# Kernel optimization log

Measured on AMD Instinct MI355X. Metric: run time of the kernel, lower is better.

## Reference

```python
import jax, jax.numpy as jnp
import numpy as np

BATCH = 2048
NUM_FIELDS = 32
EMBED = 64
NPAIRS = NUM_FIELDS * (NUM_FIELDS - 1) // 2  # 496
# static pair indices (i < j), same order as the torch double loop
ROW, COL = np.triu_indices(NUM_FIELDS, k=1)
ROW = jnp.asarray(ROW)
COL = jnp.asarray(COL)


def setup_inputs() -> dict:
    key = jax.random.key(0)
    k1, k2 = jax.random.split(key)
    emb_inputs = jax.random.normal(k1, (BATCH, NUM_FIELDS, EMBED), dtype=jnp.float32)
    # xavier_normal_ on kernel of shape (E, NC2, E): fan_in = NC2*E (dims[1:]), fan_out = E*E... 
    # torch: fan_in = size(1)*receptive = NPAIRS*EMBED? torch uses size(1)*prod(size[2:]) = NPAIRS*EMBED,
    # fan_out = size(0)*prod(size[2:]) = EMBED*EMBED; std = sqrt(2/(fan_in+fan_out))
    fan_in = NPAIRS * EMBED
    fan_out = EMBED * EMBED
    std = float(np.sqrt(2.0 / (fan_in + fan_out)))
    kernel = jax.random.normal(k2, (EMBED, NPAIRS, EMBED), dtype=jnp.float32) * std
    return {"emb_inputs": emb_inputs, "kernel": kernel}


def reference(emb_inputs, kernel):
    # emb_inputs: (B, N, E); kernel: (E, NC2, E)
    p = emb_inputs[:, ROW]  # (B, NC2, E)
    q = emb_inputs[:, COL]  # (B, NC2, E)
    # torch: kp[b,i,pair] = sum_j p[b,pair,j] * kernel[i,pair,j]; out[b,pair] = sum_i kp*q
    kp = jnp.einsum('bpj,ipj->bpi', p, kernel)  # (B, NC2, E) -- avoids (B,E,NC2,E) blowup
    outputs = jnp.sum(kp * q, axis=-1)          # (B, NC2)
    return outputs[:, None, :]                  # (B, 1, NC2)
```

## Files before the change

kernel.cpp:

```cpp
#include <hip/hip_runtime.h>
#include <hip/hip_bf16.h>
#include <math.h>

#define BATCH   2048
#define NFIELDS 32
#define EMBED   64
#define NPAIRS  496

typedef __attribute__((ext_vector_type(8))) short bf16x8;
typedef __attribute__((ext_vector_type(4))) float f32x4;

__device__ __forceinline__ unsigned short f2bf(float x) {
    unsigned int u = __float_as_uint(x);
    unsigned int r = 0x7fffu + ((u >> 16) & 1u);
    return (unsigned short)((u + r) >> 16);
}
__device__ __forceinline__ float bf2f(unsigned short b) {
    return __uint_as_float(((unsigned int)b) << 16);
}
__device__ __forceinline__ bf16x8 cvt8(const float* p) {
    float4 v0 = *(const float4*)p;
    float4 v1 = *(const float4*)(p + 4);
    bf16x8 o;
    o[0]=(short)f2bf(v0.x); o[1]=(short)f2bf(v0.y); o[2]=(short)f2bf(v0.z); o[3]=(short)f2bf(v0.w);
    o[4]=(short)f2bf(v1.x); o[5]=(short)f2bf(v1.y); o[6]=(short)f2bf(v1.z); o[7]=(short)f2bf(v1.w);
    return o;
}

__global__ __launch_bounds__(256) void convert_prepass(
    const float* __restrict__ emb, const float* __restrict__ kern,
    unsigned short* __restrict__ embT, unsigned short* __restrict__ kernB)
{
    const int EMBT4 = BATCH * NFIELDS * EMBED / 4;
    const int KER4  = EMBED * NPAIRS * EMBED / 4;
    int t = blockIdx.x * blockDim.x + threadIdx.x;
    if (t < EMBT4) {
        int j4   = t & 15;
        int rest = t >> 4;
        int b = rest & 2047;
        int f = rest >> 11;
        float4 v = *(const float4*)(emb + ((size_t)b * NFIELDS + f) * EMBED + j4 * 4);
        ushort4 o;
        o.x = f2bf(v.x); o.y = f2bf(v.y); o.z = f2bf(v.z); o.w = f2bf(v.w);
        *(ushort4*)(embT + (size_t)t * 4) = o;
    } else if (t < EMBT4 + KER4) {
        int u = t - EMBT4;
        int g    = u & 1;
        int quad = (u >> 1) & 3;
        int col  = (u >> 3) & 15;
        int blk  = (u >> 7) & 7;
        int p    = u >> 10;
        int i = (blk >> 1) * 16 + col;
        int j = (blk & 1) * 32 + quad * 8 + g * 4;
        float4 v = *(const float4*)(kern + (size_t)i * (NPAIRS*EMBED) + (size_t)p * EMBED + j);
        ushort4 o;
        o.x = f2bf(v.x); o.y = f2bf(v.y); o.z = f2bf(v.z); o.w = f2bf(v.w);
        *(ushort4*)(kernB + (size_t)u * 4) = o;
    }
}

template<bool PRE>
__global__ __launch_bounds__(256, 4) void opn_fused(
    const void* __restrict__ embP, const void* __restrict__ kernP,
    const float* __restrict__ embF, float* __restrict__ out)
{
    const int bid   = blockIdx.x;
    const int chunk = bid >> 3;
    const int bt    = bid & 7;

    const int tid  = threadIdx.x;
    const int wave = tid >> 6, lane = tid & 63;
    const int col  = lane & 15, quad = lane >> 4;
    const int pair = chunk * 4 + wave;

    int r;
    {
        float sq = sqrtf((float)(3969 - 8 * pair));
        r = (int)((63.0f - sq) * 0.5f);
        if (r > 0 && r * (63 - r) / 2 > pair) --r;
        if ((r + 1) * (63 - (r + 1)) / 2 <= pair) ++r;
    }
    const int c = r + 1 + (pair - r * (63 - r) / 2);

    __shared__ __align__(16) float Otile[256][4];

    bf16x8 kfr[4][2];
    if (PRE) {
        const unsigned short* kb = (const unsigned short*)kernP + (size_t)pair * 4096;
        #pragma unroll
        for (int nt = 0; nt < 4; ++nt)
            #pragma unroll
            for (int ks = 0; ks < 2; ++ks)
                kfr[nt][ks] = *(const bf16x8*)(kb + (nt*2 + ks) * 512 + col * 32 + quad * 8);
    } else {
        const float* kf = (const float*)kernP;
        #pragma unroll
        for (int nt = 0; nt < 4; ++nt)
            #pragma unroll
            for (int ks = 0; ks < 2; ++ks)
                kfr[nt][ks] = cvt8(kf + (size_t)(nt*16 + col) * (NPAIRS*EMBED)
                                     + (size_t)pair * EMBED + ks*32 + quad*8);
    }

    float res[16];

    #pragma unroll
    for (int it = 0; it < 16; ++it) {
        const int brow = bt * 256 + it * 16 + col;

        bf16x8 bfr0, bfr1;
        ushort4 qv[4];
        if (PRE) {
            const unsigned short* er = (const unsigned short*)embP
                                     + ((size_t)r * BATCH + brow) * EMBED;
            bfr0 = *(const bf16x8*)(er + quad*8);
            bfr1 = *(const bf16x8*)(er + 32 + quad*8);
            const unsigned short* ec = (const unsigned short*)embP
                                     + ((size_t)c * BATCH + brow) * EMBED;
            #pragma unroll
            for (int nt = 0; nt < 4; ++nt)
                qv[nt] = *(const ushort4*)(ec + nt*16 + quad*4);
        } else {
            const float* ef = (const float*)embP + ((size_t)brow * NFIELDS + r) * EMBED;
            bfr0 = cvt8(ef + quad*8);
            bfr1 = cvt8(ef + 32 + quad*8);
            const float* qp = embF + ((size_t)brow * NFIELDS + c) * EMBED + quad*4;
            #pragma unroll
            for (int nt = 0; nt < 4; ++nt) {
                f32x4 q = *(const f32x4*)(qp + nt*16);
                qv[nt].x = f2bf(q[0]); qv[nt].y = f2bf(q[1]);
                qv[nt].z = f2bf(q[2]); qv[nt].w = f2bf(q[3]);
            }
        }

        float partial = 0.f;
        #pragma unroll
        for (int nt = 0; nt < 4; ++nt) {
            f32x4 acc = {0.f, 0.f, 0.f, 0.f};
            acc = __builtin_amdgcn_mfma_f32_16x16x32_bf16(kfr[nt][0], bfr0, acc, 0, 0, 0);
            acc = __builtin_amdgcn_mfma_f32_16x16x32_bf16(kfr[nt][1], bfr1, acc, 0, 0, 0);
            partial += acc[0]*bf2f(qv[nt].x) + acc[1]*bf2f(qv[nt].y)
                     + acc[2]*bf2f(qv[nt].z) + acc[3]*bf2f(qv[nt].w);
        }
        partial += __shfl_xor(partial, 16, 64);
        partial += __shfl_xor(partial, 32, 64);
        res[it] = partial;
    }

    if (quad == 0) {
        #pragma unroll
        for (int it = 0; it < 16; ++it)
            Otile[it*16 + col][wave] = res[it];
    }
    __syncthreads();

    {
        f32x4 o = *(const f32x4*)&Otile[tid][0];
        *(f32x4*)&out[((size_t)(bt*256 + tid)) * NPAIRS + chunk*4] = o;
    }
}

extern "C" void kernel_launch(void* const* d_in, const int* in_sizes, int n_in,
                              void* d_out, int out_size, void* d_ws, size_t ws_size,
                              hipStream_t stream) {
    const float* emb  = (const float*)d_in[0];
    const float* kern = (const float*)d_in[1];
    float* out = (float*)d_out;

    const size_t embElems  = (size_t)BATCH * NFIELDS * EMBED;
    const size_t kernElems = (size_t)EMBED * NPAIRS * EMBED;
    const size_t need = (embElems + kernElems) * sizeof(unsigned short);

    if (ws_size >= need) {
        unsigned short* embT  = (unsigned short*)d_ws;
        unsigned short* kernB = embT + embElems;
        int total4 = (int)((embElems + kernElems) / 4);
        convert_prepass<<<(total4 + 255) / 256, 256, 0, stream>>>(emb, kern, embT, kernB);
        opn_fused<true><<<dim3(992), 256, 0, stream>>>(
            (const void*)embT, (const void*)kernB, emb, out);
    } else {
        opn_fused<false><<<dim3(992), 256, 0, stream>>>(
            (const void*)emb, (const void*)kern, emb, out);
    }
}
```

Measured before the change: 121.2 us.

## Double-buffer row operand via global_load_lds and halve batch tile per block

The main kernel now stages the row-field bf16 embeddings into LDS with asynchronous global_load_lds, double-buffered, and prefetches the column-field values one iteration ahead, using explicit vmcnt waits. The goal is to overlap global memory latency with the MFMA work. The batch tile per block also drops from 256 to 128 rows, which doubles the grid, and the occupancy hint rises from 4 to 6 blocks per CU to expose more parallelism. The cost is extra LDS per block and hand-written wait counts that depend on the compiler's instruction ordering. The kernel and cast-kernel loads are now repeated across twice as many blocks.

New measurement: 120.3 us. Within noise of the previous version (-0.7%).

```diff
diff --git a/kernel.cpp b/kernel.cpp
--- a/kernel.cpp
+++ b/kernel.cpp
@@ -60,13 +60,13 @@
 }
 
 template<bool PRE>
-__global__ __launch_bounds__(256, 4) void opn_fused(
+__global__ __launch_bounds__(256, 6) void opn_fused(
     const void* __restrict__ embP, const void* __restrict__ kernP,
     const float* __restrict__ embF, float* __restrict__ out)
 {
     const int bid   = blockIdx.x;
-    const int chunk = bid >> 3;
-    const int bt    = bid & 7;
+    const int chunk = bid >> 4;
+    const int bt    = bid & 15;
 
     const int tid  = threadIdx.x;
     const int wave = tid >> 6, lane = tid & 63;
@@ -82,7 +82,8 @@
     }
     const int c = r + 1 + (pair - r * (63 - r) / 2);
 
-    __shared__ __align__(16) float Otile[256][4];
+    __shared__ __align__(16) unsigned short Stage[4][2][1024];
+    __shared__ __align__(16) float Otile[128][4];
 
     bf16x8 kfr[4][2];
     if (PRE) {
@@ -102,61 +103,103 @@
                                      + (size_t)pair * EMBED + ks*32 + quad*8);
     }
 
-    float res[16];
-
-    #pragma unroll
-    for (int it = 0; it < 16; ++it) {
-        const int brow = bt * 256 + it * 16 + col;
-
-        bf16x8 bfr0, bfr1;
-        ushort4 qv[4];
-        if (PRE) {
-            const unsigned short* er = (const unsigned short*)embP
-                                     + ((size_t)r * BATCH + brow) * EMBED;
-            bfr0 = *(const bf16x8*)(er + quad*8);
-            bfr1 = *(const bf16x8*)(er + 32 + quad*8);
-            const unsigned short* ec = (const unsigned short*)embP
-                                     + ((size_t)c * BATCH + brow) * EMBED;
-            #pragma unroll
-            for (int nt = 0; nt < 4; ++nt)
-                qv[nt] = *(const ushort4*)(ec + nt*16 + quad*4);
-        } else {
+    if (PRE) {
+        const unsigned short* eb = (const unsigned short*)embP;
+        const int rr = lane & 15;
+        const int ss = lane >> 4;
+        const int brow0 = bt * 128;
+        const unsigned short* gr = eb + ((size_t)r * BATCH + brow0 + rr) * EMBED + ss*8;
+        const unsigned short* ecb = eb + ((size_t)c * BATCH + brow0 + col) * EMBED;
+        const size_t itstride = (size_t)16 * EMBED;
+
+        const unsigned offB0 = (unsigned)quad * 256 + (unsigned)col * 16;
+        const unsigned offB1 = offB0 + 1024;
+
+        #define STAGE(itv, bufv) do {                                                     \
+            const unsigned short* _r = gr + (size_t)(itv) * itstride;                     \
+            __builtin_amdgcn_global_load_lds(                                             \
+                (const __attribute__((address_space(1))) void*)_r,                        \
+                (__attribute__((address_space(3))) void*)&Stage[wave][bufv][0],   16, 0, 0); \
+            __builtin_amdgcn_global_load_lds(                                             \
+                (const __attribute__((address_space(1))) void*)(_r + 32),                 \
+                (__attribute__((address_space(3))) void*)&Stage[wave][bufv][512], 16, 0, 0); \
+        } while (0)
+
+        #define LOADQ(dst, itv) do {                                                      \
+            const unsigned short* _e = ecb + (size_t)(itv) * itstride;                    \
+            dst##0 = *(const ushort4*)(_e + 0*16 + quad*4);                               \
+            dst##1 = *(const ushort4*)(_e + 1*16 + quad*4);                               \
+            dst##2 = *(const ushort4*)(_e + 2*16 + quad*4);                               \
+            dst##3 = *(const ushort4*)(_e + 3*16 + quad*4);                               \
+        } while (0)
+
+        ushort4 qA0, qA1, qA2, qA3, qB0, qB1, qB2, qB3;
+        STAGE(0, 0);
+        LOADQ(qA, 0);
+
+        #pragma unroll
+        for (int it = 0; it < 8; ++it) {
+            const int buf = it & 1;
+            if (it < 7) {
+                STAGE(it + 1, buf ^ 1);
+                if ((it & 1) == 0) { LOADQ(qB, it + 1); }
+                else               { LOADQ(qA, it + 1); }
+                asm volatile("s_waitcnt vmcnt(6)" ::: "memory");
+            } else {
+                asm volatile("s_waitcnt vmcnt(0)" ::: "memory");
+            }
+            __builtin_amdgcn_sched_barrier(0);
+
+            const char* rb = (const char*)&Stage[wave][buf][0];
+            bf16x8 bfr0 = *(const bf16x8*)(rb + offB0);
+            bf16x8 bfr1 = *(const bf16x8*)(rb + offB1);
+
+            float partial = 0.f;
+            #pragma unroll
+            for (int nt = 0; nt < 4; ++nt) {
+                f32x4 acc = {0.f, 0.f, 0.f, 0.f};
+                acc = __builtin_amdgcn_mfma_f32_16x16x32_bf16(kfr[nt][0], bfr0, acc, 0, 0, 0);
+                acc = __builtin_amdgcn_mfma_f32_16x16x32_bf16(kfr[nt][1], bfr1, acc, 0, 0, 0);
+                ushort4 qv;
+                if ((it & 1) == 0) qv = (nt == 0) ? qA0 : (nt == 1) ? qA1 : (nt == 2) ? qA2 : qA3;
+                else               qv = (nt == 0) ? qB0 : (nt == 1) ? qB1 : (nt == 2) ? qB2 : qB3;
+                partial += acc[0]*bf2f(qv.x) + acc[1]*bf2f(qv.y)
+                         + acc[2]*bf2f(qv.z) + acc[3]*bf2f(qv.w);
+            }
+            partial += __shfl_xor(partial, 16, 64);
+            partial += __shfl_xor(partial, 32, 64);
+            if (quad == 0) Otile[it*16 + col][wave] = partial;
+        }
+        #undef STAGE
+        #undef LOADQ
+    } else {
+        #pragma unroll
+        for (int it = 0; it < 8; ++it) {
+            const int brow = bt * 128 + it * 16 + col;
             const float* ef = (const float*)embP + ((size_t)brow * NFIELDS + r) * EMBED;
-            bfr0 = cvt8(ef + quad*8);
-            bfr1 = cvt8(ef + 32 + quad*8);
+            bf16x8 bfr0 = cvt8(ef + quad*8);
+            bf16x8 bfr1 = cvt8(ef + 32 + quad*8);
             const float* qp = embF + ((size_t)brow * NFIELDS + c) * EMBED + quad*4;
+            float partial = 0.f;
             #pragma unroll
             for (int nt = 0; nt < 4; ++nt) {
                 f32x4 q = *(const f32x4*)(qp + nt*16);
-                qv[nt].x = f2bf(q[0]); qv[nt].y = f2bf(q[1]);
-                qv[nt].z = f2bf(q[2]); qv[nt].w = f2bf(q[3]);
+                f32x4 acc = {0.f, 0.f, 0.f, 0.f};
+                acc = __builtin_amdgcn_mfma_f32_16x16x32_bf16(kfr[nt][0], bfr0, acc, 0, 0, 0);
+                acc = __builtin_amdgcn_mfma_f32_16x16x32_bf16(kfr[nt][1], bfr1, acc, 0, 0, 0);
+                partial += acc[0]*q[0] + acc[1]*q[1] + acc[2]*q[2] + acc[3]*q[3];
             }
+            partial += __shfl_xor(partial, 16, 64);
+            partial += __shfl_xor(partial, 32, 64);
+            if (quad == 0) Otile[it*16 + col][wave] = partial;
         }
-
-        float partial = 0.f;
-        #pragma unroll
-        for (int nt = 0; nt < 4; ++nt) {
-            f32x4 acc = {0.f, 0.f, 0.f, 0.f};
-            acc = __builtin_amdgcn_mfma_f32_16x16x32_bf16(kfr[nt][0], bfr0, acc, 0, 0, 0);
-            acc = __builtin_amdgcn_mfma_f32_16x16x32_bf16(kfr[nt][1], bfr1, acc, 0, 0, 0);
-            partial += acc[0]*bf2f(qv[nt].x) + acc[1]*bf2f(qv[nt].y)
-                     + acc[2]*bf2f(qv[nt].z) + acc[3]*bf2f(qv[nt].w);
-        }
-        partial += __shfl_xor(partial, 16, 64);
-        partial += __shfl_xor(partial, 32, 64);
-        res[it] = partial;
-    }
-
-    if (quad == 0) {
-        #pragma unroll
-        for (int it = 0; it < 16; ++it)
-            Otile[it*16 + col][wave] = res[it];
-    }
+    }
+
     __syncthreads();
 
-    {
+    if (tid < 128) {
         f32x4 o = *(const f32x4*)&Otile[tid][0];
-        *(f32x4*)&out[((size_t)(bt*256 + tid)) * NPAIRS + chunk*4] = o;
+        *(f32x4*)&out[((size_t)(bt*128 + tid)) * NPAIRS + chunk*4] = o;
     }
 }
 
@@ -176,10 +219,10 @@
         unsigned short* kernB = embT + embElems;
         int total4 = (int)((embElems + kernElems) / 4);
         convert_prepass<<<(total4 + 255) / 256, 256, 0, stream>>>(emb, kern, embT, kernB);
-        opn_fused<true><<<dim3(992), 256, 0, stream>>>(
+        opn_fused<true><<<dim3(1984), 256, 0, stream>>>(
             (const void*)embT, (const void*)kernB, emb, out);
     } else {
-        opn_fused<false><<<dim3(992), 256, 0, stream>>>(
+        opn_fused<false><<<dim3(1984), 256, 0, stream>>>(
             (const void*)emb, (const void*)kern, emb, out);
     }
 }
```
